# Performance work log

Measured on AMD Instinct MI355X. Metric: run time of the kernel, lower is better.

## Reference

```python
import jax, jax.numpy as jnp
import numpy as np

B, IN_SHAPE, EXP_SHAPE, HID, NB_CLASSES = 64, 10000, 53, 1500, 2048


def setup_inputs() -> dict:
    key = jax.random.key(0)
    ks = jax.random.split(key, 8)
    gos = jax.random.uniform(ks[0], (B, IN_SHAPE), dtype=jnp.float32)
    exp_x = jax.random.uniform(ks[1], (B, EXP_SHAPE), dtype=jnp.float32)
    # FlatModel params (torch Linear: y = x @ W.T + b; store pre-transposed)
    W1 = jax.random.normal(ks[2], (IN_SHAPE, HID), dtype=jnp.float32) * (1.0 / np.sqrt(IN_SHAPE))
    b1 = jnp.zeros((HID,), dtype=jnp.float32)
    W2 = jax.random.normal(ks[3], (HID + EXP_SHAPE, NB_CLASSES), dtype=jnp.float32) * (1.0 / np.sqrt(HID + EXP_SHAPE))
    b2 = jnp.zeros((NB_CLASSES,), dtype=jnp.float32)
    # HPO adjacency (non-trainable buffer in the original; values in [0,1))
    hpo_matrix = jax.random.uniform(ks[4], (NB_CLASSES, NB_CLASSES), dtype=jnp.float32)
    return {"gos": gos, "exp_x": exp_x, "W1": W1, "b1": b1, "W2": W2, "b2": b2, "hpo_matrix": hpo_matrix}


def reference(gos, exp_x, W1, b1, W2, b2, hpo_matrix):
    # FlatModel (eval mode: dropout is identity). torch F.gelu default = exact erf gelu.
    h = jax.nn.gelu(gos @ W1 + b1, approximate=False)          # (B, HID)
    x = jnp.concatenate([h, exp_x], axis=1)                     # (B, HID+EXP)
    flat = jax.nn.sigmoid(x @ W2 + b2)                          # (B, C)
    # HPOLayer + permute + MaxPool1d(C): out[b,j] = max_i flat[b,j] * M[i,j]
    out = jnp.max(flat[:, None, :] * hpo_matrix[None, :, :], axis=1)  # (B, C)
    return out
```

## Files before the change

kernel.cpp:

```cpp
#include <hip/hip_runtime.h>
#include <math.h>

#define B64 64
#define IN_SH 10000
#define GOSLD 10240
#define EXP_SH 53
#define HID 1500
#define NPAD1 1536
#define NBC 2048
#define K2 1553
#define XLD 1664
#define KS1 40
#define KCH1 256
#define KST1 8
#define KS2 13
#define KCH2 128
#define KST2 4
#define CMCH 32
#define ACCF (NPAD1 * B64 + NBC * B64)

using short8  = __attribute__((ext_vector_type(8))) short;
using floatx4 = __attribute__((ext_vector_type(4))) float;
using uintx4  = __attribute__((ext_vector_type(4))) unsigned int;

__device__ __forceinline__ unsigned short f2bf(float f) {
    unsigned u = __float_as_uint(f);
    u += 0x7fffu + ((u >> 16) & 1u);
    return (unsigned short)(u >> 16);
}

__global__ __launch_bounds__(256) void pre_k(const float* __restrict__ g,
                                             unsigned short* __restrict__ gb,
                                             const float* __restrict__ M,
                                             float* __restrict__ cm,
                                             float* __restrict__ accz) {
    int bi = blockIdx.x;
    if (bi < 320) {
        int idx = bi * 256 + threadIdx.x;
        int b = idx / (GOSLD / 8);
        int k = (idx % (GOSLD / 8)) * 8;
        unsigned int o[4] = {0u, 0u, 0u, 0u};
        if (k < IN_SH) {
            const float* p = g + (size_t)b * IN_SH + k;
            #pragma unroll
            for (int i = 0; i < 4; i++) {
                float lo = p[2 * i], hi = p[2 * i + 1];
                o[i] = (unsigned)f2bf(lo) | ((unsigned)f2bf(hi) << 16);
            }
        }
        uintx4 v; v.x = o[0]; v.y = o[1]; v.z = o[2]; v.w = o[3];
        *(uintx4*)(gb + (size_t)b * GOSLD + k) = v;
    } else if (bi < 576) {
        int ci = bi - 320;
        int j  = (ci & 7) * 256 + threadIdx.x;
        int i0 = (ci >> 3) * 64;
        float m = 0.0f;
        #pragma unroll 16
        for (int i = i0; i < i0 + 64; i++)
            m = fmaxf(m, M[(size_t)i * NBC + j]);
        cm[(ci >> 3) * NBC + j] = m;
    } else {
        int t = (bi - 576) * 256 + threadIdx.x;
        floatx4 z = (floatx4){0.f, 0.f, 0.f, 0.f};
        #pragma unroll
        for (int i = 0; i < 28; i++)
            *(floatx4*)(accz + (size_t)(i * 2048 + t) * 4) = z;
    }
}

__device__ __forceinline__ void load_step(
    const float* __restrict__ W, const unsigned short* __restrict__ brow0,
    int kb, int K, int ldw, int ldb, int cW, bool nok,
    float wv[8], uintx4 bv[4])
{
    #pragma unroll
    for (int j = 0; j < 8; j++) {
        int k = kb + j;
        wv[j] = (nok && k < K) ? W[(size_t)k * ldw + cW] : 0.f;
    }
    #pragma unroll
    for (int s = 0; s < 4; s++)
        bv[s] = *(const uintx4*)(brow0 + (size_t)s * 16 * ldb + kb);
}

template<int KSTEPS>
__global__ __launch_bounds__(256) void mfma_gemm(
    const float* __restrict__ W, const unsigned short* __restrict__ Bm,
    float* __restrict__ accbuf, int N, int K, int ldw, int ldb, int kchunk)
{
    int tid  = threadIdx.x;
    int w    = tid >> 6;
    int lane = tid & 63;
    int q    = lane >> 4;
    int l15  = lane & 15;
    int n0   = blockIdx.x * 64;
    int k0   = blockIdx.y * kchunk;
    int cW   = n0 + 16 * w + l15;
    bool nok = cW < N;
    int qk   = q * 8;

    floatx4 acc[4];
    #pragma unroll
    for (int s = 0; s < 4; s++) acc[s] = (floatx4){0.f, 0.f, 0.f, 0.f};

    const unsigned short* brow0 = Bm + (size_t)l15 * ldb;

    float  wv[2][8];
    uintx4 bv[2][4];
    load_step(W, brow0, k0 + qk, K, ldw, ldb, cW, nok, wv[0], bv[0]);
    if (KSTEPS > 1)
        load_step(W, brow0, k0 + 32 + qk, K, ldw, ldb, cW, nok, wv[1], bv[1]);

    #pragma unroll
    for (int st = 0; st < KSTEPS; st++) {
        const int p = st & 1;
        float  wt[8];
        uintx4 bt[4];
        if (st + 2 < KSTEPS)
            load_step(W, brow0, k0 + (st + 2) * 32 + qk, K, ldw, ldb, cW, nok, wt, bt);

        short8 af;
        #pragma unroll
        for (int j = 0; j < 8; j++) af[j] = (short)f2bf(wv[p][j]);
        #pragma unroll
        for (int s = 0; s < 4; s++) {
            short8 bf8 = __builtin_bit_cast(short8, bv[p][s]);
            acc[s] = __builtin_amdgcn_mfma_f32_16x16x32_bf16(af, bf8, acc[s], 0, 0, 0);
        }

        if (st + 2 < KSTEPS) {
            #pragma unroll
            for (int j = 0; j < 8; j++) wv[p][j] = wt[j];
            #pragma unroll
            for (int s = 0; s < 4; s++) bv[p][s] = bt[s];
        }
    }

    int nrow = n0 + 16 * w + q * 4;
    #pragma unroll
    for (int s = 0; s < 4; s++) {
        #pragma unroll
        for (int r = 0; r < 4; r++)
            atomicAdd(&accbuf[(size_t)(nrow + r) * 64 + s * 16 + l15], acc[s][r]);
    }
}

__global__ __launch_bounds__(256) void combine1(
    const float* __restrict__ hpre, const float* __restrict__ b1,
    const float* __restrict__ expx, unsigned short* __restrict__ X)
{
    int idx = blockIdx.x * 256 + threadIdx.x;
    int b = idx & 63;
    int n = idx >> 6;
    float v = 0.f;
    if (n < HID) {
        float s = hpre[(size_t)n * 64 + b] + b1[n];
        v = 0.5f * s * (1.0f + erff(s * 0.70710678118654752f));
    } else if (n < HID + EXP_SH) {
        v = expx[b * EXP_SH + (n - HID)];
    }
    X[(size_t)b * XLD + n] = f2bf(v);
}

__global__ __launch_bounds__(256) void final_k(
    const float* __restrict__ logits, const float* __restrict__ b2,
    const float* __restrict__ cm, float* __restrict__ out)
{
    int idx = blockIdx.x * 256 + threadIdx.x;
    int b = idx & 63;
    int j = idx >> 6;
    float s = logits[(size_t)j * 64 + b] + b2[j];
    float sig = 1.0f / (1.0f + expf(-s));
    float m = 0.f;
    #pragma unroll
    for (int c = 0; c < CMCH; c++) m = fmaxf(m, cm[c * NBC + j]);
    out[(size_t)b * NBC + j] = sig * m;
}

extern "C" void kernel_launch(void* const* d_in, const int* in_sizes, int n_in,
                              void* d_out, int out_size, void* d_ws, size_t ws_size,
                              hipStream_t stream) {
    const float* gos  = (const float*)d_in[0];
    const float* expx = (const float*)d_in[1];
    const float* W1   = (const float*)d_in[2];
    const float* b1   = (const float*)d_in[3];
    const float* W2   = (const float*)d_in[4];
    const float* b2   = (const float*)d_in[5];
    const float* hpo  = (const float*)d_in[6];
    float* out = (float*)d_out;

    char* ws = (char*)d_ws;
    unsigned short* gosB = (unsigned short*)ws;
    float* hpre   = (float*)(ws + 1310720);
    float* logits = (float*)(ws + 1310720 + 393216);
    unsigned short* X = (unsigned short*)(ws + 1310720 + 393216 + 524288);
    float* cm = (float*)(ws + 1310720 + 393216 + 524288 + 212992);

    pre_k<<<584, 256, 0, stream>>>(gos, gosB, hpo, cm, hpre);

    mfma_gemm<KST1><<<dim3(NPAD1 / 64, KS1), 256, 0, stream>>>(
        W1, gosB, hpre, HID, IN_SH, HID, GOSLD, KCH1);

    combine1<<<(B64 * XLD) / 256, 256, 0, stream>>>(hpre, b1, expx, X);

    mfma_gemm<KST2><<<dim3(NBC / 64, KS2), 256, 0, stream>>>(
        W2, X, logits, NBC, K2, NBC, XLD, KCH2);

    final_k<<<(B64 * NBC) / 256, 256, 0, stream>>>(logits, b2, cm, out);
}
```

Measured before the change: 167.6 us.

## Pre-swizzle bf16 activation operands into MFMA fragment order and deepen prefetch

The bf16 copies of the activations (gos and the hidden/exp concat) are now written in an MFMA-fragment-ordered layout, so each lane reads its B operand from a contiguous, fully coalesced 16-byte slot instead of strided row loads. The GEMM prefetch pipeline goes from two stages to three register-buffered stages to hide more load latency. combine1 now produces eight outputs per thread in the swizzled order, with a smaller grid. The added prefetch depth raises register pressure and may reduce occupancy.

```diff
diff --git a/kernel.cpp b/kernel.cpp
--- a/kernel.cpp
+++ b/kernel.cpp
@@ -3,21 +3,18 @@
 
 #define B64 64
 #define IN_SH 10000
-#define GOSLD 10240
 #define EXP_SH 53
 #define HID 1500
 #define NPAD1 1536
 #define NBC 2048
 #define K2 1553
-#define XLD 1664
 #define KS1 40
-#define KCH1 256
 #define KST1 8
 #define KS2 13
-#define KCH2 128
 #define KST2 4
+#define NSTEP1 320
+#define NSTEP2 52
 #define CMCH 32
-#define ACCF (NPAD1 * B64 + NBC * B64)
 
 using short8  = __attribute__((ext_vector_type(8))) short;
 using floatx4 = __attribute__((ext_vector_type(4))) float;
@@ -29,27 +26,32 @@
     return (unsigned short)(u >> 16);
 }
 
-__global__ __launch_bounds__(256) void pre_k(const float* __restrict__ g,
-                                             unsigned short* __restrict__ gb,
-                                             const float* __restrict__ M,
-                                             float* __restrict__ cm,
-                                             float* __restrict__ accz) {
+
+__global__ __launch_bounds__(256) void prep_k(const float* __restrict__ g,
+                                              unsigned short* __restrict__ gosBf,
+                                              const float* __restrict__ M,
+                                              float* __restrict__ cm,
+                                              float* __restrict__ accz) {
     int bi = blockIdx.x;
     if (bi < 320) {
-        int idx = bi * 256 + threadIdx.x;
-        int b = idx / (GOSLD / 8);
-        int k = (idx % (GOSLD / 8)) * 8;
-        unsigned int o[4] = {0u, 0u, 0u, 0u};
-        if (k < IN_SH) {
-            const float* p = g + (size_t)b * IN_SH + k;
-            #pragma unroll
-            for (int i = 0; i < 4; i++) {
-                float lo = p[2 * i], hi = p[2 * i + 1];
-                o[i] = (unsigned)f2bf(lo) | ((unsigned)f2bf(hi) << 16);
-            }
+        int t    = bi * 256 + threadIdx.x;
+        int lane = t & 63;
+        int sgrp = (t >> 6) & 3;
+        int step = t >> 8;
+        int q    = lane >> 4;
+        int l15  = lane & 15;
+        int b    = sgrp * 16 + l15;
+        int k0   = step * 32 + q * 8;
+        const float* p = g + (size_t)b * IN_SH + k0;
+        unsigned int o[4];
+        #pragma unroll
+        for (int i = 0; i < 4; i++) {
+            float lo = (k0 + 2 * i     < IN_SH) ? p[2 * i]     : 0.f;
+            float hi = (k0 + 2 * i + 1 < IN_SH) ? p[2 * i + 1] : 0.f;
+            o[i] = (unsigned)f2bf(lo) | ((unsigned)f2bf(hi) << 16);
         }
         uintx4 v; v.x = o[0]; v.y = o[1]; v.z = o[2]; v.w = o[3];
-        *(uintx4*)(gb + (size_t)b * GOSLD + k) = v;
+        *(uintx4*)(gosBf + (size_t)t * 8) = v;
     } else if (bi < 576) {
         int ci = bi - 320;
         int j  = (ci & 7) * 256 + threadIdx.x;
@@ -68,56 +70,60 @@
     }
 }
 
-__device__ __forceinline__ void load_step(
-    const float* __restrict__ W, const unsigned short* __restrict__ brow0,
-    int kb, int K, int ldw, int ldb, int cW, bool nok,
-    float wv[8], uintx4 bv[4])
-{
+__device__ __forceinline__ void load_w8(const float* __restrict__ W, int kb, int K,
+                                        int ldw, int cW, bool nok, float wv[8]) {
     #pragma unroll
     for (int j = 0; j < 8; j++) {
         int k = kb + j;
         wv[j] = (nok && k < K) ? W[(size_t)k * ldw + cW] : 0.f;
     }
+}
+__device__ __forceinline__ void load_b4(const unsigned short* __restrict__ bf,
+                                        int stg, uintx4 bv[4]) {
     #pragma unroll
     for (int s = 0; s < 4; s++)
-        bv[s] = *(const uintx4*)(brow0 + (size_t)s * 16 * ldb + kb);
+        bv[s] = *(const uintx4*)(bf + (size_t)(stg * 4 + s) * 512);
 }
 
 template<int KSTEPS>
-__global__ __launch_bounds__(256) void mfma_gemm(
-    const float* __restrict__ W, const unsigned short* __restrict__ Bm,
-    float* __restrict__ accbuf, int N, int K, int ldw, int ldb, int kchunk)
-{
-    int tid  = threadIdx.x;
+__device__ __forceinline__ void gemm_core(
+    const float* __restrict__ W, const unsigned short* __restrict__ Bf,
+    float* __restrict__ accbuf, int N, int K, int ldw, int bx, int by, int tid)
+{
     int w    = tid >> 6;
     int lane = tid & 63;
     int q    = lane >> 4;
     int l15  = lane & 15;
-    int n0   = blockIdx.x * 64;
-    int k0   = blockIdx.y * kchunk;
+    int n0   = bx * 64;
+    int k0   = by * (KSTEPS * 32);
     int cW   = n0 + 16 * w + l15;
     bool nok = cW < N;
     int qk   = q * 8;
 
+    const unsigned short* bf = Bf + (size_t)(by * KSTEPS * 4) * 512 + (size_t)lane * 8;
+
     floatx4 acc[4];
     #pragma unroll
     for (int s = 0; s < 4; s++) acc[s] = (floatx4){0.f, 0.f, 0.f, 0.f};
 
-    const unsigned short* brow0 = Bm + (size_t)l15 * ldb;
-
-    float  wv[2][8];
-    uintx4 bv[2][4];
-    load_step(W, brow0, k0 + qk, K, ldw, ldb, cW, nok, wv[0], bv[0]);
-    if (KSTEPS > 1)
-        load_step(W, brow0, k0 + 32 + qk, K, ldw, ldb, cW, nok, wv[1], bv[1]);
+    float  wv[3][8];
+    uintx4 bv[3][4];
+    #pragma unroll
+    for (int d = 0; d < 3; d++) {
+        int st = (d < KSTEPS) ? d : KSTEPS - 1;
+        load_w8(W, k0 + st * 32 + qk, K, ldw, cW, nok, wv[d]);
+        load_b4(bf, st, bv[d]);
+    }
 
     #pragma unroll
     for (int st = 0; st < KSTEPS; st++) {
-        const int p = st & 1;
+        const int p = st % 3;
         float  wt[8];
         uintx4 bt[4];
-        if (st + 2 < KSTEPS)
-            load_step(W, brow0, k0 + (st + 2) * 32 + qk, K, ldw, ldb, cW, nok, wt, bt);
+        if (st + 3 < KSTEPS) {
+            load_w8(W, k0 + (st + 3) * 32 + qk, K, ldw, cW, nok, wt);
+            load_b4(bf, st + 3, bt);
+        }
 
         short8 af;
         #pragma unroll
@@ -128,7 +134,7 @@
             acc[s] = __builtin_amdgcn_mfma_f32_16x16x32_bf16(af, bf8, acc[s], 0, 0, 0);
         }
 
-        if (st + 2 < KSTEPS) {
+        if (st + 3 < KSTEPS) {
             #pragma unroll
             for (int j = 0; j < 8; j++) wv[p][j] = wt[j];
             #pragma unroll
@@ -145,21 +151,52 @@
     }
 }
 
+__global__ __launch_bounds__(256) void gemm1_k(
+    const float* __restrict__ W1, const unsigned short* __restrict__ gosBf,
+    float* __restrict__ hpre)
+{
+    gemm_core<KST1>(W1, gosBf, hpre, HID, IN_SH, HID, blockIdx.x, blockIdx.y, threadIdx.x);
+}
+
+__global__ __launch_bounds__(256) void gemm2_k(
+    const float* __restrict__ W2, const unsigned short* __restrict__ Xf,
+    float* __restrict__ logits)
+{
+    gemm_core<KST2>(W2, Xf, logits, NBC, K2, NBC, blockIdx.x, blockIdx.y, threadIdx.x);
+}
+
 __global__ __launch_bounds__(256) void combine1(
     const float* __restrict__ hpre, const float* __restrict__ b1,
-    const float* __restrict__ expx, unsigned short* __restrict__ X)
-{
-    int idx = blockIdx.x * 256 + threadIdx.x;
-    int b = idx & 63;
-    int n = idx >> 6;
-    float v = 0.f;
-    if (n < HID) {
-        float s = hpre[(size_t)n * 64 + b] + b1[n];
-        v = 0.5f * s * (1.0f + erff(s * 0.70710678118654752f));
-    } else if (n < HID + EXP_SH) {
-        v = expx[b * EXP_SH + (n - HID)];
-    }
-    X[(size_t)b * XLD + n] = f2bf(v);
+    const float* __restrict__ expx, unsigned short* __restrict__ Xf)
+{
+    int t    = blockIdx.x * 256 + threadIdx.x;
+    int lane = t & 63;
+    int sgrp = (t >> 6) & 3;
+    int step = t >> 8;
+    int q    = lane >> 4;
+    int l15  = lane & 15;
+    int b    = sgrp * 16 + l15;
+    int kb   = step * 32 + q * 8;
+    unsigned int o[4];
+    #pragma unroll
+    for (int i = 0; i < 4; i++) {
+        unsigned int lohi[2];
+        #pragma unroll
+        for (int h = 0; h < 2; h++) {
+            int n = kb + 2 * i + h;
+            float v = 0.f;
+            if (n < HID) {
+                float s = hpre[(size_t)n * 64 + b] + b1[n];
+                v = 0.5f * s * (1.0f + erff(s * 0.70710678118654752f));
+            } else if (n < HID + EXP_SH) {
+                v = expx[b * EXP_SH + (n - HID)];
+            }
+            lohi[h] = f2bf(v);
+        }
+        o[i] = lohi[0] | (lohi[1] << 16);
+    }
+    uintx4 v; v.x = o[0]; v.y = o[1]; v.z = o[2]; v.w = o[3];
+    *(uintx4*)(Xf + (size_t)t * 8) = v;
 }
 
 __global__ __launch_bounds__(256) void final_k(
@@ -190,21 +227,19 @@
     float* out = (float*)d_out;
 
     char* ws = (char*)d_ws;
-    unsigned short* gosB = (unsigned short*)ws;
+    unsigned short* gosBf = (unsigned short*)ws;
     float* hpre   = (float*)(ws + 1310720);
     float* logits = (float*)(ws + 1310720 + 393216);
-    unsigned short* X = (unsigned short*)(ws + 1310720 + 393216 + 524288);
+    unsigned short* Xf = (unsigned short*)(ws + 1310720 + 393216 + 524288);
     float* cm = (float*)(ws + 1310720 + 393216 + 524288 + 212992);
 
-    pre_k<<<584, 256, 0, stream>>>(gos, gosB, hpo, cm, hpre);
-
-    mfma_gemm<KST1><<<dim3(NPAD1 / 64, KS1), 256, 0, stream>>>(
-        W1, gosB, hpre, HID, IN_SH, HID, GOSLD, KCH1);
-
-    combine1<<<(B64 * XLD) / 256, 256, 0, stream>>>(hpre, b1, expx, X);
-
-    mfma_gemm<KST2><<<dim3(NBC / 64, KS2), 256, 0, stream>>>(
-        W2, X, logits, NBC, K2, NBC, XLD, KCH2);
+    prep_k<<<584, 256, 0, stream>>>(gos, gosBf, hpo, cm, hpre);
+
+    gemm1_k<<<dim3(NPAD1 / 64, KS1), 256, 0, stream>>>(W1, gosBf, hpre);
+
+    combine1<<<52, 256, 0, stream>>>(hpre, b1, expx, Xf);
+
+    gemm2_k<<<dim3(NBC / 64, KS2), 256, 0, stream>>>(W2, Xf, logits);
 
     final_k<<<(B64 * NBC) / 256, 256, 0, stream>>>(logits, b2, cm, out);
 }
```

Measured after the change: 162.7 us. 3.0% less time.
